# Kernel optimization log

Measured on AMD Instinct MI355X. Metric: run time of the kernel, lower is better.

## Reference

```python
import jax, jax.numpy as jnp
import numpy as np

N = 4096
D = 256
H = 8
HD = D // H
EPS = 1e-5
NEG = -1e9


def layer_norm(x, g, b):
    mu = jnp.mean(x, axis=-1, keepdims=True)
    var = jnp.mean(jnp.square(x - mu), axis=-1, keepdims=True)
    return (x - mu) * jax.lax.rsqrt(var + EPS) * g + b


def setup_inputs() -> dict:
    key = jax.random.key(0)
    ks = jax.random.split(key, 12)
    s = 1.0 / np.sqrt(D)
    inp = {
        "x": jax.random.normal(ks[0], (N, D), dtype=jnp.float32),
        "adj": jax.random.randint(ks[1], (N, N), 0, 2, dtype=jnp.int32),
        "Wq": jax.random.uniform(ks[2], (D, D), jnp.float32, -s, s),
        "Wk": jax.random.uniform(ks[3], (D, D), jnp.float32, -s, s),
        "Wv": jax.random.uniform(ks[4], (D, D), jnp.float32, -s, s),
        "bq": jnp.zeros((D,), jnp.float32),
        "bk": jnp.zeros((D,), jnp.float32),
        "bv": jnp.zeros((D,), jnp.float32),
        "Wo": jax.random.uniform(ks[5], (D, D), jnp.float32, -s, s),
        "bo": jnp.zeros((D,), jnp.float32),
        "g1": jnp.ones((D,), jnp.float32),
        "beta1": jnp.zeros((D,), jnp.float32),
        "W1": jax.random.uniform(ks[6], (2 * D, D), jnp.float32, -s, s),
        "b1": jnp.zeros((2 * D,), jnp.float32),
        "W2": jax.random.uniform(ks[7], (D, 2 * D), jnp.float32, -1.0 / np.sqrt(2 * D), 1.0 / np.sqrt(2 * D)),
        "b2": jnp.zeros((D,), jnp.float32),
        "g2": jnp.ones((D,), jnp.float32),
        "beta2": jnp.zeros((D,), jnp.float32),
    }
    return inp


def reference(x, adj, Wq, Wk, Wv, bq, bk, bv, Wo, bo, g1, beta1, W1, b1, W2, b2, g2, beta2):
    n = adj.shape[0]
    # allowed = adj + I > 0 ; attention only over neighbors + self-loop
    allowed = (adj + jnp.eye(n, dtype=adj.dtype)) > 0  # (n, n) bool

    q = (x @ Wq.T + bq).reshape(n, H, HD)
    k = (x @ Wk.T + bk).reshape(n, H, HD)
    v = (x @ Wv.T + bv).reshape(n, H, HD)

    scale = 1.0 / np.sqrt(HD)
    scores = jnp.einsum('nhd,mhd->hnm', q, k) * scale  # (H, n, n)
    scores = jnp.where(allowed[None, :, :], scores, NEG)
    attn = jax.nn.softmax(scores, axis=-1)
    o = jnp.einsum('hnm,mhd->nhd', attn, v).reshape(n, D)
    h = o @ Wo.T + bo

    x = layer_norm(x + h, g1, beta1)
    ffn = jax.nn.relu(x @ W1.T + b1) @ W2.T + b2
    x = layer_norm(x + ffn, g2, beta2)
    return x
```

## Files before the change

### kernel.cpp

```cpp
#include <hip/hip_runtime.h>
#include <hip/hip_bf16.h>

typedef __attribute__((ext_vector_type(4))) float f32x4;
typedef __attribute__((ext_vector_type(8))) short s16x8;

#define NROWS 4096
#define DMODEL 256
#define NHEAD 8
#define HDIM 32
#define PSTRIDE 72
#define OSTRIDE 33
#define M2C 24.0f
#define NM (NROWS * DMODEL)

__device__ __forceinline__ short bf16r(float f) {
    union { float f; unsigned u; } v; v.f = f;
    unsigned r = v.u + 0x7fffu + ((v.u >> 16) & 1u);
    return (short)(r >> 16);
}

__device__ __forceinline__ float fexp2(float x) {
    float r;
    asm("v_exp_f32 %0, %1" : "=v"(r) : "v"(x));
    return r;
}

__device__ __forceinline__ unsigned pk_bf16(float a, float b) {
#if __has_builtin(__builtin_amdgcn_cvt_pk_bf16_f32)
    typedef __bf16 bf2 __attribute__((ext_vector_type(2)));
    union { bf2 h; unsigned u; } c;
    c.h = __builtin_amdgcn_cvt_pk_bf16_f32(a, b);
    return c.u;
#else
    return (unsigned)(unsigned short)bf16r(a) | ((unsigned)(unsigned short)bf16r(b) << 16);
#endif
}

__device__ __forceinline__ s16x8 pack8(float4 a, float4 b) {
    s16x8 r;
    r[0] = bf16r(a.x); r[1] = bf16r(a.y); r[2] = bf16r(a.z); r[3] = bf16r(a.w);
    r[4] = bf16r(b.x); r[5] = bf16r(b.y); r[6] = bf16r(b.z); r[7] = bf16r(b.w);
    return r;
}

__global__ __launch_bounds__(256) void prep_kernel(const int* __restrict__ adj,
                                                   unsigned* __restrict__ mask,
                                                   const float* __restrict__ Wq,
                                                   const float* __restrict__ Wk,
                                                   const float* __restrict__ Wv,
                                                   const float* __restrict__ Wo,
                                                   const float* __restrict__ W1,
                                                   const float* __restrict__ W2,
                                                   short* __restrict__ wout) {
    const int lane = threadIdx.x & 63;
    if (blockIdx.x < 2048) {
        const int waveid = blockIdx.x * 4 + (threadIdx.x >> 6);
#pragma unroll
        for (int i = 0; i < 32; ++i) {
            const int task = waveid + i * 8192;
            const int row = task >> 6, chunk = task & 63;
            const int c = chunk * 64 + lane;
            int a = adj[(size_t)row * NROWS + c];
            unsigned long long m = __ballot(a > 0 || c == row);
            if (lane == 0)      mask[row * 128 + chunk * 2]     = (unsigned)m;
            else if (lane == 1) mask[row * 128 + chunk * 2 + 1] = (unsigned)(m >> 32);
        }
    } else {
        int i = ((blockIdx.x - 2048) * 256 + threadIdx.x) * 8;
        const float* src; int off;
        if (i < 262144) {
            const float* ws[4] = {Wq, Wk, Wv, Wo};
            src = ws[i >> 16]; off = i & 65535;
        } else if (i < 393216) { src = W1; off = i - 262144; }
        else                   { src = W2; off = i - 393216; }
        float4 a = *(const float4*)(src + off);
        float4 b = *(const float4*)(src + off + 4);
        *(s16x8*)(wout + i) = pack8(a, b);
    }
}

__global__ __launch_bounds__(256) void qkv_kernel(const float* __restrict__ X,
                                                  const short* __restrict__ Wb,
                                                  const float* __restrict__ bq,
                                                  const float* __restrict__ bk,
                                                  const float* __restrict__ bv,
                                                  short* __restrict__ Qb,
                                                  short* __restrict__ Kb,
                                                  short* __restrict__ Vtb) {
    const int tid = threadIdx.x;
    const int wv = tid >> 6, lane = tid & 63;
    const int quad = lane >> 4, col = lane & 15;
    const int n0 = blockIdx.x * 64 + wv * 16;
    const int o0 = blockIdx.y * 64;
    const int z = o0 >> 8;
    const float* bias = (z == 0) ? bq : (z == 1 ? bk : bv);
    const float QSC = 0.25505653437397888f;

    f32x4 zero = {0.f, 0.f, 0.f, 0.f};
    f32x4 acc[4] = {zero, zero, zero, zero};
    const float* ap = X + (size_t)(n0 + col) * DMODEL + quad * 8;
    const short* wp = Wb + (size_t)(o0 + col) * DMODEL + quad * 8;
#pragma unroll
    for (int k0 = 0; k0 < DMODEL; k0 += 32) {
        float4 a0 = *(const float4*)(ap + k0);
        float4 a1 = *(const float4*)(ap + k0 + 4);
        s16x8 af = pack8(a0, a1);
#pragma unroll
        for (int t = 0; t < 4; ++t) {
            s16x8 bf = *(const s16x8*)(wp + (size_t)t * 16 * DMODEL + k0);
            acc[t] = __builtin_amdgcn_mfma_f32_16x16x32_bf16(af, bf, acc[t], 0, 0, 0);
        }
    }
#pragma unroll
    for (int t = 0; t < 4; ++t) {
        const int o = o0 + t * 16 + col;
        const int oo = o & 255;
        float bvv = bias[oo];
#pragma unroll
        for (int r = 0; r < 4; ++r) {
            int n = n0 + quad * 4 + r;
            float v = acc[t][r] + bvv;
            if (z == 0)      Qb[(size_t)n * DMODEL + oo] = bf16r(v * QSC);
            else if (z == 1) Kb[(size_t)(oo >> 5) * NROWS * HDIM + (size_t)n * HDIM + (oo & 31)] = bf16r(v);
            else             Vtb[(size_t)oo * NROWS + n] = bf16r(v);
        }
    }
}

__global__ __launch_bounds__(256) void attn_kernel(const short* __restrict__ Qb,
                                                   const short* __restrict__ Kb,
                                                   const short* __restrict__ Vtb,
                                                   const unsigned* __restrict__ mask,
                                                   float* __restrict__ Opart,
                                                   float* __restrict__ lpart) {
    __shared__ union {
        short sP[2][16 * PSTRIDE];
        float sO[HDIM][OSTRIDE];
    } u[4];
    __shared__ float sl[4][32];

    const int tid = threadIdx.x;
    const int wv = tid >> 6, lane = tid & 63;
    const int quad = lane >> 4, col = lane & 15;
    const int khalf = blockIdx.x & 1;
    const int h = (blockIdx.x >> 1) & 7;
    const int q0 = (blockIdx.x >> 4) * 32;
    const int kw = khalf * 2048 + wv * 512;

    s16x8 qf[2];
    qf[0] = *(const s16x8*)(Qb + (size_t)(q0 + col) * DMODEL + h * HDIM + quad * 8);
    qf[1] = *(const s16x8*)(Qb + (size_t)(q0 + 16 + col) * DMODEL + h * HDIM + quad * 8);

    const short* kp  = Kb + (size_t)h * NROWS * HDIM + (size_t)(kw + col) * HDIM + quad * 8;
    const short* vp0 = Vtb + (size_t)(h * HDIM + col) * NROWS + kw + quad * 8;
    const short* vp1 = vp0 + (size_t)16 * NROWS;
    const unsigned* mp0 = mask + (size_t)(q0 + col) * 128 + (kw >> 5);
    const unsigned* mp1 = mp0 + 16 * 128;

    const short onev = (col == 0) ? (short)0x3F80 : (short)0;
    const s16x8 ones = {onev, onev, onev, onev, onev, onev, onev, onev};

    f32x4 zero = {0.f, 0.f, 0.f, 0.f};
    f32x4 acc[2][2] = {{zero, zero}, {zero, zero}};
    f32x4 lacc[2] = {zero, zero};
    const f32x4 cinit = {-M2C, -M2C, -M2C, -M2C};

    auto loadK = [&](int it, s16x8* kf, uint2* w0, uint2* w1) {
        const short* k = kp + it * 64 * HDIM;
        kf[0] = *(const s16x8*)(k);
        kf[1] = *(const s16x8*)(k + 16 * HDIM);
        kf[2] = *(const s16x8*)(k + 32 * HDIM);
        kf[3] = *(const s16x8*)(k + 48 * HDIM);
        *w0 = *(const uint2*)(mp0 + it * 2);
        *w1 = *(const uint2*)(mp1 + it * 2);
    };

    auto proc = [&](const s16x8* kf, uint2 w0, uint2 w1, int it) {
        const short* v0 = vp0 + it * 64;
        const short* v1 = vp1 + it * 64;
        s16x8 vf00 = *(const s16x8*)(v0);
        s16x8 vf01 = *(const s16x8*)(v0 + 32);
        s16x8 vf10 = *(const s16x8*)(v1);
        s16x8 vf11 = *(const s16x8*)(v1 + 32);
#pragma unroll
        for (int qs = 0; qs < 2; ++qs) {
            unsigned wlo = (qs ? w1.x : w0.x) >> (quad * 4);
            unsigned whi = (qs ? w1.y : w0.y) >> (quad * 4);
            f32x4 st[4];
            st[0] = __builtin_amdgcn_mfma_f32_16x16x32_bf16(kf[0], qf[qs], cinit, 0, 0, 0);
            st[1] = __builtin_amdgcn_mfma_f32_16x16x32_bf16(kf[1], qf[qs], cinit, 0, 0, 0);
            st[2] = __builtin_amdgcn_mfma_f32_16x16x32_bf16(kf[2], qf[qs], cinit, 0, 0, 0);
            st[3] = __builtin_amdgcn_mfma_f32_16x16x32_bf16(kf[3], qf[qs], cinit, 0, 0, 0);

            float p[4][4];
#pragma unroll
            for (int t = 0; t < 4; ++t) {
                unsigned wm = (t < 2) ? wlo : whi;
#pragma unroll
                for (int r = 0; r < 4; ++r) {
                    float e = fexp2(st[t][r]);
                    bool ok = (wm & (1u << ((t & 1) * 16 + r))) != 0u;
                    p[t][r] = ok ? e : 0.f;
                }
            }

            short* pb = &u[wv].sP[qs][0];
#pragma unroll
            for (int t = 0; t < 4; ++t) {
                uint2 pr;
                pr.x = pk_bf16(p[t][0], p[t][1]);
                pr.y = pk_bf16(p[t][2], p[t][3]);
                *(uint2*)(pb + col * PSTRIDE + t * 16 + quad * 4) = pr;
            }
            s16x8 pb0 = *(const s16x8*)(pb + col * PSTRIDE + quad * 8);
            s16x8 pb1 = *(const s16x8*)(pb + col * PSTRIDE + 32 + quad * 8);

            acc[qs][0] = __builtin_amdgcn_mfma_f32_16x16x32_bf16(vf00, pb0, acc[qs][0], 0, 0, 0);
            acc[qs][0] = __builtin_amdgcn_mfma_f32_16x16x32_bf16(vf01, pb1, acc[qs][0], 0, 0, 0);
            acc[qs][1] = __builtin_amdgcn_mfma_f32_16x16x32_bf16(vf10, pb0, acc[qs][1], 0, 0, 0);
            acc[qs][1] = __builtin_amdgcn_mfma_f32_16x16x32_bf16(vf11, pb1, acc[qs][1], 0, 0, 0);
            lacc[qs] = __builtin_amdgcn_mfma_f32_16x16x32_bf16(ones, pb0, lacc[qs], 0, 0, 0);
            lacc[qs] = __builtin_amdgcn_mfma_f32_16x16x32_bf16(ones, pb1, lacc[qs], 0, 0, 0);
        }
    };

    s16x8 kfA[4], kfB[4];
    uint2 w0A, w1A, w0B, w1B;
    loadK(0, kfA, &w0A, &w1A);
    for (int it = 0; it < 8; it += 2) {
        loadK(it + 1, kfB, &w0B, &w1B);
        proc(kfA, w0A, w1A, it);
        if (it < 6) loadK(it + 2, kfA, &w0A, &w1A);
        proc(kfB, w0B, w1B, it + 1);
    }

#pragma unroll
    for (int qs = 0; qs < 2; ++qs) {
        if (lane < 16) sl[wv][qs * 16 + col] = lacc[qs][0];
#pragma unroll
        for (int rr = 0; rr < 4; ++rr) {
            u[wv].sO[quad * 4 + rr][qs * 16 + col]      = acc[qs][0][rr];
            u[wv].sO[16 + quad * 4 + rr][qs * 16 + col] = acc[qs][1][rr];
        }
    }
    __syncthreads();

    const int q = tid >> 3, hd0 = (tid & 7) * 4;
    float l = sl[0][q] + sl[1][q] + sl[2][q] + sl[3][q];
    float4 ov;
    ov.x = u[0].sO[hd0][q]     + u[1].sO[hd0][q]     + u[2].sO[hd0][q]     + u[3].sO[hd0][q];
    ov.y = u[0].sO[hd0 + 1][q] + u[1].sO[hd0 + 1][q] + u[2].sO[hd0 + 1][q] + u[3].sO[hd0 + 1][q];
    ov.z = u[0].sO[hd0 + 2][q] + u[1].sO[hd0 + 2][q] + u[2].sO[hd0 + 2][q] + u[3].sO[hd0 + 2][q];
    ov.w = u[0].sO[hd0 + 3][q] + u[1].sO[hd0 + 3][q] + u[2].sO[hd0 + 3][q] + u[3].sO[hd0 + 3][q];
    *(float4*)(Opart + (size_t)khalf * NM + (size_t)(q0 + q) * DMODEL + h * HDIM + hd0) = ov;
    if ((tid & 7) == 0) lpart[khalf * NROWS * NHEAD + (q0 + q) * NHEAD + h] = l;
}

template<int K, bool RELU, bool B16OUT>
__device__ __forceinline__ void gemm_body(const short* __restrict__ A,
                                          const short* __restrict__ W,
                                          const float* __restrict__ bias,
                                          float* __restrict__ Cf,
                                          short* __restrict__ Cb,
                                          int Ocols) {
    const int tid = threadIdx.x;
    const int wv = tid >> 6, lane = tid & 63;
    const int quad = lane >> 4, col = lane & 15;
    const int n0 = blockIdx.x * 64 + wv * 16;
    const int o0 = blockIdx.y * 64;
    f32x4 zero = {0.f, 0.f, 0.f, 0.f};
    f32x4 acc[4] = {zero, zero, zero, zero};
    const short* ap = A + (size_t)(n0 + col) * K + quad * 8;
    const short* wp = W + (size_t)(o0 + col) * K + quad * 8;
#pragma unroll
    for (int k0 = 0; k0 < K; k0 += 32) {
        s16x8 af = *(const s16x8*)(ap + k0);
#pragma unroll
        for (int t = 0; t < 4; ++t) {
            s16x8 bf = *(const s16x8*)(wp + (size_t)t * 16 * K + k0);
            acc[t] = __builtin_amdgcn_mfma_f32_16x16x32_bf16(af, bf, acc[t], 0, 0, 0);
        }
    }
#pragma unroll
    for (int t = 0; t < 4; ++t) {
        const int o = o0 + t * 16 + col;
        float bvv = bias[o];
#pragma unroll
        for (int r = 0; r < 4; ++r) {
            int n = n0 + quad * 4 + r;
            float v = acc[t][r] + bvv;
            if (RELU) v = fmaxf(v, 0.f);
            if (B16OUT) Cb[(size_t)n * Ocols + o] = bf16r(v);
            else        Cf[(size_t)n * Ocols + o] = v;
        }
    }
}

__global__ __launch_bounds__(256) void gemm_w1(const short* __restrict__ A,
                                               const short* __restrict__ W,
                                               const float* __restrict__ bias,
                                               short* __restrict__ Cb) {
    gemm_body<256, true, true>(A, W, bias, nullptr, Cb, 512);
}

__global__ __launch_bounds__(256) void gemm_w2(const short* __restrict__ A,
                                               const short* __restrict__ W,
                                               const float* __restrict__ bias,
                                               float* __restrict__ Cf) {
    gemm_body<512, false, false>(A, W, bias, Cf, nullptr, 256);
}

__global__ __launch_bounds__(256) void gemm_wo(const float* __restrict__ Opart,
                                               const float* __restrict__ lpart,
                                               const short* __restrict__ W,
                                               const float* __restrict__ bias,
                                               float* __restrict__ Cf) {
    const int tid = threadIdx.x;
    const int wv = tid >> 6, lane = tid & 63;
    const int quad = lane >> 4, col = lane & 15;
    const int n0 = blockIdx.x * 64 + wv * 16;
    const int o0 = blockIdx.y * 64;
    f32x4 zero = {0.f, 0.f, 0.f, 0.f};
    f32x4 acc[4] = {zero, zero, zero, zero};
    const int n = n0 + col;
    const float* a0p = Opart + (size_t)n * DMODEL + quad * 8;
    const float* a1p = a0p + NM;
    const float* l0p = lpart + (size_t)n * NHEAD;
    const float* l1p = l0p + NROWS * NHEAD;
    const short* wp = W + (size_t)(o0 + col) * DMODEL + quad * 8;
#pragma unroll
    for (int k0 = 0; k0 < DMODEL; k0 += 32) {
        const int head = k0 >> 5;
        float inv = 1.f / (l0p[head] + l1p[head]);
        float4 xa = *(const float4*)(a0p + k0);
        float4 xb = *(const float4*)(a0p + k0 + 4);
        float4 ya = *(const float4*)(a1p + k0);
        float4 yb = *(const float4*)(a1p + k0 + 4);
        float4 s0, s1;
        s0.x = (xa.x + ya.x) * inv; s0.y = (xa.y + ya.y) * inv;
        s0.z = (xa.z + ya.z) * inv; s0.w = (xa.w + ya.w) * inv;
        s1.x = (xb.x + yb.x) * inv; s1.y = (xb.y + yb.y) * inv;
        s1.z = (xb.z + yb.z) * inv; s1.w = (xb.w + yb.w) * inv;
        s16x8 af = pack8(s0, s1);
#pragma unroll
        for (int t = 0; t < 4; ++t) {
            s16x8 bf = *(const s16x8*)(wp + (size_t)t * 16 * DMODEL + k0);
            acc[t] = __builtin_amdgcn_mfma_f32_16x16x32_bf16(af, bf, acc[t], 0, 0, 0);
        }
    }
#pragma unroll
    for (int t = 0; t < 4; ++t) {
        const int o = o0 + t * 16 + col;
        float bvv = bias[o];
#pragma unroll
        for (int r = 0; r < 4; ++r)
            Cf[(size_t)(n0 + quad * 4 + r) * DMODEL + o] = acc[t][r] + bvv;
    }
}

__global__ __launch_bounds__(256) void ln_kernel(const float* __restrict__ Xa,
                                                 const float* __restrict__ Xb,
                                                 const float* __restrict__ g,
                                                 const float* __restrict__ be,
                                                 float* __restrict__ Y,
                                                 short* __restrict__ Yb) {
    const int wv = threadIdx.x >> 6, lane = threadIdx.x & 63;
    const int row = blockIdx.x * 4 + wv;
    const float4 av = *(const float4*)(Xa + (size_t)row * DMODEL + lane * 4);
    const float4 bv = *(const float4*)(Xb + (size_t)row * DMODEL + lane * 4);
    float v0 = av.x + bv.x, v1 = av.y + bv.y, v2 = av.z + bv.z, v3 = av.w + bv.w;
    float s = v0 + v1 + v2 + v3;
#pragma unroll
    for (int m = 1; m < 64; m <<= 1) s += __shfl_xor(s, m, 64);
    float mean = s * (1.f / 256.f);
    float d0 = v0 - mean, d1 = v1 - mean, d2 = v2 - mean, d3 = v3 - mean;
    float q = d0 * d0 + d1 * d1 + d2 * d2 + d3 * d3;
#pragma unroll
    for (int m = 1; m < 64; m <<= 1) q += __shfl_xor(q, m, 64);
    float rstd = rsqrtf(q * (1.f / 256.f) + 1e-5f);
    const float4 gv  = *(const float4*)(g + lane * 4);
    const float4 bev = *(const float4*)(be + lane * 4);
    float4 y;
    y.x = d0 * rstd * gv.x + bev.x;
    y.y = d1 * rstd * gv.y + bev.y;
    y.z = d2 * rstd * gv.z + bev.z;
    y.w = d3 * rstd * gv.w + bev.w;
    *(float4*)(Y + (size_t)row * DMODEL + lane * 4) = y;
    if (Yb) {
        uint2 yb;
        yb.x = pk_bf16(y.x, y.y);
        yb.y = pk_bf16(y.z, y.w);
        *(uint2*)(Yb + (size_t)row * DMODEL + lane * 4) = yb;
    }
}

extern "C" void kernel_launch(void* const* d_in, const int* in_sizes, int n_in,
                              void* d_out, int out_size, void* d_ws, size_t ws_size,
                              hipStream_t stream) {
    const float* x   = (const float*)d_in[0];
    const int*   adj = (const int*)d_in[1];
    const float* Wq  = (const float*)d_in[2];
    const float* Wk  = (const float*)d_in[3];
    const float* Wv  = (const float*)d_in[4];
    const float* bq  = (const float*)d_in[5];
    const float* bk  = (const float*)d_in[6];
    const float* bv  = (const float*)d_in[7];
    const float* Wo  = (const float*)d_in[8];
    const float* bo  = (const float*)d_in[9];
    const float* g1  = (const float*)d_in[10];
    const float* be1 = (const float*)d_in[11];
    const float* W1  = (const float*)d_in[12];
    const float* b1  = (const float*)d_in[13];
    const float* W2  = (const float*)d_in[14];
    const float* b2  = (const float*)d_in[15];
    const float* g2  = (const float*)d_in[16];
    const float* be2 = (const float*)d_in[17];
    float* out = (float*)d_out;

    char* p = (char*)d_ws;
    unsigned* mask = (unsigned*)p; p += (size_t)NROWS * 128 * 4;
    short* Wb    = (short*)p;      p += (size_t)524288 * 2;
    short* Qb    = (short*)p;      p += (size_t)NM * 2;
    short* Kb    = (short*)p;      p += (size_t)NM * 2;
    short* Vtb   = (short*)p;      p += (size_t)NM * 2;
    float* Opart = (float*)p;      p += (size_t)2 * NM * 4;
    float* lpart = (float*)p;      p += (size_t)2 * NROWS * NHEAD * 4;
    float* hbuf  = (float*)p;      p += (size_t)NM * 4;
    float* y1    = (float*)p;      p += (size_t)NM * 4;
    short* y1b   = (short*)p;      p += (size_t)NM * 2;
    short* rbuf  = (short*)p;      p += (size_t)NROWS * 512 * 2;
    float* t2    = Opart;

    prep_kernel<<<dim3(2304), dim3(256), 0, stream>>>(adj, mask, Wq, Wk, Wv, Wo, W1, W2, Wb);
    qkv_kernel<<<dim3(64, 12), dim3(256), 0, stream>>>(x, Wb, bq, bk, bv, Qb, Kb, Vtb);
    attn_kernel<<<dim3(2048), dim3(256), 0, stream>>>(Qb, Kb, Vtb, mask, Opart, lpart);
    gemm_wo<<<dim3(64, 4), dim3(256), 0, stream>>>(Opart, lpart, Wb + 196608, bo, hbuf);
    ln_kernel<<<dim3(1024), dim3(256), 0, stream>>>(x, hbuf, g1, be1, y1, y1b);
    gemm_w1<<<dim3(64, 8), dim3(256), 0, stream>>>(y1b, Wb + 262144, b1, rbuf);
    gemm_w2<<<dim3(64, 4), dim3(256), 0, stream>>>(rbuf, Wb + 393216, b2, t2);
    ln_kernel<<<dim3(1024), dim3(256), 0, stream>>>(y1, t2, g2, be2, out, nullptr);
}
```

Measured before the change: 261.1 us.

## Shrink GEMM output tiles to 16 columns for more blocks; simplify attention loop

Measured after the change: 288.9 us. 1.11x slower.

```diff
diff --git a/kernel.cpp b/kernel.cpp
--- a/kernel.cpp
+++ b/kernel.cpp
@@ -90,40 +90,36 @@
     const int tid = threadIdx.x;
     const int wv = tid >> 6, lane = tid & 63;
     const int quad = lane >> 4, col = lane & 15;
-    const int n0 = blockIdx.x * 64 + wv * 16;
-    const int o0 = blockIdx.y * 64;
+    const int n0 = (blockIdx.x * 4 + wv) * 16;
+    const int o0 = blockIdx.y * 16;
     const int z = o0 >> 8;
     const float* bias = (z == 0) ? bq : (z == 1 ? bk : bv);
     const float QSC = 0.25505653437397888f;
 
-    f32x4 zero = {0.f, 0.f, 0.f, 0.f};
-    f32x4 acc[4] = {zero, zero, zero, zero};
+    f32x4 acc0 = {0.f, 0.f, 0.f, 0.f}, acc1 = {0.f, 0.f, 0.f, 0.f};
     const float* ap = X + (size_t)(n0 + col) * DMODEL + quad * 8;
     const short* wp = Wb + (size_t)(o0 + col) * DMODEL + quad * 8;
 #pragma unroll
-    for (int k0 = 0; k0 < DMODEL; k0 += 32) {
+    for (int k0 = 0; k0 < DMODEL; k0 += 64) {
         float4 a0 = *(const float4*)(ap + k0);
         float4 a1 = *(const float4*)(ap + k0 + 4);
-        s16x8 af = pack8(a0, a1);
-#pragma unroll
-        for (int t = 0; t < 4; ++t) {
-            s16x8 bf = *(const s16x8*)(wp + (size_t)t * 16 * DMODEL + k0);
-            acc[t] = __builtin_amdgcn_mfma_f32_16x16x32_bf16(af, bf, acc[t], 0, 0, 0);
-        }
-    }
-#pragma unroll
-    for (int t = 0; t < 4; ++t) {
-        const int o = o0 + t * 16 + col;
-        const int oo = o & 255;
-        float bvv = bias[oo];
-#pragma unroll
-        for (int r = 0; r < 4; ++r) {
-            int n = n0 + quad * 4 + r;
-            float v = acc[t][r] + bvv;
-            if (z == 0)      Qb[(size_t)n * DMODEL + oo] = bf16r(v * QSC);
-            else if (z == 1) Kb[(size_t)(oo >> 5) * NROWS * HDIM + (size_t)n * HDIM + (oo & 31)] = bf16r(v);
-            else             Vtb[(size_t)oo * NROWS + n] = bf16r(v);
-        }
+        float4 a2 = *(const float4*)(ap + k0 + 32);
+        float4 a3 = *(const float4*)(ap + k0 + 36);
+        s16x8 b0 = *(const s16x8*)(wp + k0);
+        s16x8 b1 = *(const s16x8*)(wp + k0 + 32);
+        acc0 = __builtin_amdgcn_mfma_f32_16x16x32_bf16(pack8(a0, a1), b0, acc0, 0, 0, 0);
+        acc1 = __builtin_amdgcn_mfma_f32_16x16x32_bf16(pack8(a2, a3), b1, acc1, 0, 0, 0);
+    }
+    const int o = o0 + col;
+    const int oo = o & 255;
+    float bvv = bias[oo];
+#pragma unroll
+    for (int r = 0; r < 4; ++r) {
+        int n = n0 + quad * 4 + r;
+        float v = acc0[r] + acc1[r] + bvv;
+        if (z == 0)      Qb[(size_t)n * DMODEL + oo] = bf16r(v * QSC);
+        else if (z == 1) Kb[(size_t)(oo >> 5) * NROWS * HDIM + (size_t)n * HDIM + (oo & 31)] = bf16r(v);
+        else             Vtb[(size_t)oo * NROWS + n] = bf16r(v);
     }
 }
 
@@ -165,32 +161,31 @@
     f32x4 lacc[2] = {zero, zero};
     const f32x4 cinit = {-M2C, -M2C, -M2C, -M2C};
 
-    auto loadK = [&](int it, s16x8* kf, uint2* w0, uint2* w1) {
+#pragma unroll 2
+    for (int it = 0; it < 8; ++it) {
         const short* k = kp + it * 64 * HDIM;
-        kf[0] = *(const s16x8*)(k);
-        kf[1] = *(const s16x8*)(k + 16 * HDIM);
-        kf[2] = *(const s16x8*)(k + 32 * HDIM);
-        kf[3] = *(const s16x8*)(k + 48 * HDIM);
-        *w0 = *(const uint2*)(mp0 + it * 2);
-        *w1 = *(const uint2*)(mp1 + it * 2);
-    };
-
-    auto proc = [&](const s16x8* kf, uint2 w0, uint2 w1, int it) {
+        s16x8 kf0 = *(const s16x8*)(k);
+        s16x8 kf1 = *(const s16x8*)(k + 16 * HDIM);
+        s16x8 kf2 = *(const s16x8*)(k + 32 * HDIM);
+        s16x8 kf3 = *(const s16x8*)(k + 48 * HDIM);
+        uint2 w0 = *(const uint2*)(mp0 + it * 2);
+        uint2 w1 = *(const uint2*)(mp1 + it * 2);
         const short* v0 = vp0 + it * 64;
         const short* v1 = vp1 + it * 64;
         s16x8 vf00 = *(const s16x8*)(v0);
         s16x8 vf01 = *(const s16x8*)(v0 + 32);
         s16x8 vf10 = *(const s16x8*)(v1);
         s16x8 vf11 = *(const s16x8*)(v1 + 32);
+
 #pragma unroll
         for (int qs = 0; qs < 2; ++qs) {
             unsigned wlo = (qs ? w1.x : w0.x) >> (quad * 4);
             unsigned whi = (qs ? w1.y : w0.y) >> (quad * 4);
             f32x4 st[4];
-            st[0] = __builtin_amdgcn_mfma_f32_16x16x32_bf16(kf[0], qf[qs], cinit, 0, 0, 0);
-            st[1] = __builtin_amdgcn_mfma_f32_16x16x32_bf16(kf[1], qf[qs], cinit, 0, 0, 0);
-            st[2] = __builtin_amdgcn_mfma_f32_16x16x32_bf16(kf[2], qf[qs], cinit, 0, 0, 0);
-            st[3] = __builtin_amdgcn_mfma_f32_16x16x32_bf16(kf[3], qf[qs], cinit, 0, 0, 0);
+            st[0] = __builtin_amdgcn_mfma_f32_16x16x32_bf16(kf0, qf[qs], cinit, 0, 0, 0);
+            st[1] = __builtin_amdgcn_mfma_f32_16x16x32_bf16(kf1, qf[qs], cinit, 0, 0, 0);
+            st[2] = __builtin_amdgcn_mfma_f32_16x16x32_bf16(kf2, qf[qs], cinit, 0, 0, 0);
+            st[3] = __builtin_amdgcn_mfma_f32_16x16x32_bf16(kf3, qf[qs], cinit, 0, 0, 0);
 
             float p[4][4];
 #pragma unroll
@@ -222,16 +217,6 @@
             lacc[qs] = __builtin_amdgcn_mfma_f32_16x16x32_bf16(ones, pb0, lacc[qs], 0, 0, 0);
             lacc[qs] = __builtin_amdgcn_mfma_f32_16x16x32_bf16(ones, pb1, lacc[qs], 0, 0, 0);
         }
-    };
-
-    s16x8 kfA[4], kfB[4];
-    uint2 w0A, w1A, w0B, w1B;
-    loadK(0, kfA, &w0A, &w1A);
-    for (int it = 0; it < 8; it += 2) {
-        loadK(it + 1, kfB, &w0B, &w1B);
-        proc(kfA, w0A, w1A, it);
-        if (it < 6) loadK(it + 2, kfA, &w0A, &w1A);
-        proc(kfB, w0B, w1B, it + 1);
     }
 
 #pragma unroll
@@ -257,42 +242,38 @@
 }
 
 template<int K, bool RELU, bool B16OUT>
-__device__ __forceinline__ void gemm_body(const short* __restrict__ A,
-                                          const short* __restrict__ W,
-                                          const float* __restrict__ bias,
-                                          float* __restrict__ Cf,
-                                          short* __restrict__ Cb,
-                                          int Ocols) {
+__device__ __forceinline__ void gemm16_body(const short* __restrict__ A,
+                                            const short* __restrict__ W,
+                                            const float* __restrict__ bias,
+                                            float* __restrict__ Cf,
+                                            short* __restrict__ Cb,
+                                            int Ocols) {
     const int tid = threadIdx.x;
     const int wv = tid >> 6, lane = tid & 63;
     const int quad = lane >> 4, col = lane & 15;
-    const int n0 = blockIdx.x * 64 + wv * 16;
-    const int o0 = blockIdx.y * 64;
-    f32x4 zero = {0.f, 0.f, 0.f, 0.f};
-    f32x4 acc[4] = {zero, zero, zero, zero};
+    const int n0 = (blockIdx.x * 4 + wv) * 16;
+    const int o0 = blockIdx.y * 16;
+    f32x4 acc0 = {0.f, 0.f, 0.f, 0.f}, acc1 = {0.f, 0.f, 0.f, 0.f};
     const short* ap = A + (size_t)(n0 + col) * K + quad * 8;
     const short* wp = W + (size_t)(o0 + col) * K + quad * 8;
 #pragma unroll
-    for (int k0 = 0; k0 < K; k0 += 32) {
-        s16x8 af = *(const s16x8*)(ap + k0);
-#pragma unroll
-        for (int t = 0; t < 4; ++t) {
-            s16x8 bf = *(const s16x8*)(wp + (size_t)t * 16 * K + k0);
-            acc[t] = __builtin_amdgcn_mfma_f32_16x16x32_bf16(af, bf, acc[t], 0, 0, 0);
-        }
-    }
-#pragma unroll
-    for (int t = 0; t < 4; ++t) {
-        const int o = o0 + t * 16 + col;
-        float bvv = bias[o];
-#pragma unroll
-        for (int r = 0; r < 4; ++r) {
-            int n = n0 + quad * 4 + r;
-            float v = acc[t][r] + bvv;
-            if (RELU) v = fmaxf(v, 0.f);
-            if (B16OUT) Cb[(size_t)n * Ocols + o] = bf16r(v);
-            else        Cf[(size_t)n * Ocols + o] = v;
-        }
+    for (int k0 = 0; k0 < K; k0 += 64) {
+        s16x8 a0 = *(const s16x8*)(ap + k0);
+        s16x8 b0 = *(const s16x8*)(wp + k0);
+        s16x8 a1 = *(const s16x8*)(ap + k0 + 32);
+        s16x8 b1 = *(const s16x8*)(wp + k0 + 32);
+        acc0 = __builtin_amdgcn_mfma_f32_16x16x32_bf16(a0, b0, acc0, 0, 0, 0);
+        acc1 = __builtin_amdgcn_mfma_f32_16x16x32_bf16(a1, b1, acc1, 0, 0, 0);
+    }
+    const int o = o0 + col;
+    float bvv = bias[o];
+#pragma unroll
+    for (int r = 0; r < 4; ++r) {
+        int n = n0 + quad * 4 + r;
+        float v = acc0[r] + acc1[r] + bvv;
+        if (RELU) v = fmaxf(v, 0.f);
+        if (B16OUT) Cb[(size_t)n * Ocols + o] = bf16r(v);
+        else        Cf[(size_t)n * Ocols + o] = v;
     }
 }
 
@@ -300,14 +281,14 @@
                                                const short* __restrict__ W,
                                                const float* __restrict__ bias,
                                                short* __restrict__ Cb) {
-    gemm_body<256, true, true>(A, W, bias, nullptr, Cb, 512);
+    gemm16_body<256, true, true>(A, W, bias, nullptr, Cb, 512);
 }
 
 __global__ __launch_bounds__(256) void gemm_w2(const short* __restrict__ A,
                                                const short* __restrict__ W,
                                                const float* __restrict__ bias,
                                                float* __restrict__ Cf) {
-    gemm_body<512, false, false>(A, W, bias, Cf, nullptr, 256);
+    gemm16_body<512, false, false>(A, W, bias, Cf, nullptr, 256);
 }
 
 __global__ __launch_bounds__(256) void gemm_wo(const float* __restrict__ Opart,
@@ -318,10 +299,9 @@
     const int tid = threadIdx.x;
     const int wv = tid >> 6, lane = tid & 63;
     const int quad = lane >> 4, col = lane & 15;
-    const int n0 = blockIdx.x * 64 + wv * 16;
-    const int o0 = blockIdx.y * 64;
-    f32x4 zero = {0.f, 0.f, 0.f, 0.f};
-    f32x4 acc[4] = {zero, zero, zero, zero};
+    const int n0 = (blockIdx.x * 4 + wv) * 16;
+    const int o0 = blockIdx.y * 16;
+    f32x4 acc0 = {0.f, 0.f, 0.f, 0.f}, acc1 = {0.f, 0.f, 0.f, 0.f};
     const int n = n0 + col;
     const float* a0p = Opart + (size_t)n * DMODEL + quad * 8;
     const float* a1p = a0p + NM;
@@ -342,20 +322,15 @@
         s1.x = (xb.x + yb.x) * inv; s1.y = (xb.y + yb.y) * inv;
         s1.z = (xb.z + yb.z) * inv; s1.w = (xb.w + yb.w) * inv;
         s16x8 af = pack8(s0, s1);
-#pragma unroll
-        for (int t = 0; t < 4; ++t) {
-            s16x8 bf = *(const s16x8*)(wp + (size_t)t * 16 * DMODEL + k0);
-            acc[t] = __builtin_amdgcn_mfma_f32_16x16x32_bf16(af, bf, acc[t], 0, 0, 0);
-        }
-    }
-#pragma unroll
-    for (int t = 0; t < 4; ++t) {
-        const int o = o0 + t * 16 + col;
-        float bvv = bias[o];
-#pragma unroll
-        for (int r = 0; r < 4; ++r)
-            Cf[(size_t)(n0 + quad * 4 + r) * DMODEL + o] = acc[t][r] + bvv;
-    }
+        s16x8 bf = *(const s16x8*)(wp + k0);
+        if (head & 1) acc1 = __builtin_amdgcn_mfma_f32_16x16x32_bf16(af, bf, acc1, 0, 0, 0);
+        else          acc0 = __builtin_amdgcn_mfma_f32_16x16x32_bf16(af, bf, acc0, 0, 0, 0);
+    }
+    const int o = o0 + col;
+    float bvv = bias[o];
+#pragma unroll
+    for (int r = 0; r < 4; ++r)
+        Cf[(size_t)(n0 + quad * 4 + r) * DMODEL + o] = acc0[r] + acc1[r] + bvv;
 }
 
 __global__ __launch_bounds__(256) void ln_kernel(const float* __restrict__ Xa,
@@ -432,11 +407,11 @@
     float* t2    = Opart;
 
     prep_kernel<<<dim3(2304), dim3(256), 0, stream>>>(adj, mask, Wq, Wk, Wv, Wo, W1, W2, Wb);
-    qkv_kernel<<<dim3(64, 12), dim3(256), 0, stream>>>(x, Wb, bq, bk, bv, Qb, Kb, Vtb);
+    qkv_kernel<<<dim3(64, 48), dim3(256), 0, stream>>>(x, Wb, bq, bk, bv, Qb, Kb, Vtb);
     attn_kernel<<<dim3(2048), dim3(256), 0, stream>>>(Qb, Kb, Vtb, mask, Opart, lpart);
-    gemm_wo<<<dim3(64, 4), dim3(256), 0, stream>>>(Opart, lpart, Wb + 196608, bo, hbuf);
+    gemm_wo<<<dim3(64, 16), dim3(256), 0, stream>>>(Opart, lpart, Wb + 196608, bo, hbuf);
     ln_kernel<<<dim3(1024), dim3(256), 0, stream>>>(x, hbuf, g1, be1, y1, y1b);
-    gemm_w1<<<dim3(64, 8), dim3(256), 0, stream>>>(y1b, Wb + 262144, b1, rbuf);
-    gemm_w2<<<dim3(64, 4), dim3(256), 0, stream>>>(rbuf, Wb + 393216, b2, t2);
+    gemm_w1<<<dim3(64, 32), dim3(256), 0, stream>>>(y1b, Wb + 262144, b1, rbuf);
+    gemm_w2<<<dim3(64, 16), dim3(256), 0, stream>>>(rbuf, Wb + 393216, b2, t2);
     ln_kernel<<<dim3(1024), dim3(256), 0, stream>>>(y1, t2, g2, be2, out, nullptr);
 }
```

## Fuse post-attention GEMMs and layernorms into one kernel; merge QKV with prep

Applied to the files above, without the earlier changes.

New measurement: 240.8 us. -7.8%, faster.

```diff
diff --git a/kernel.cpp b/kernel.cpp
--- a/kernel.cpp
+++ b/kernel.cpp
@@ -12,6 +12,10 @@
 #define OSTRIDE 33
 #define M2C 24.0f
 #define NM (NROWS * DMODEL)
+#define SA_S 264
+#define SH_S 268
+#define SY_S 264
+#define SR_S 520
 
 __device__ __forceinline__ short bf16r(float f) {
     union { float f; unsigned u; } v; v.f = f;
@@ -43,18 +47,62 @@
     return r;
 }
 
-__global__ __launch_bounds__(256) void prep_kernel(const int* __restrict__ adj,
-                                                   unsigned* __restrict__ mask,
-                                                   const float* __restrict__ Wq,
-                                                   const float* __restrict__ Wk,
-                                                   const float* __restrict__ Wv,
-                                                   const float* __restrict__ Wo,
-                                                   const float* __restrict__ W1,
-                                                   const float* __restrict__ W2,
-                                                   short* __restrict__ wout) {
-    const int lane = threadIdx.x & 63;
-    if (blockIdx.x < 2048) {
-        const int waveid = blockIdx.x * 4 + (threadIdx.x >> 6);
+__global__ __launch_bounds__(256) void qkvprep_kernel(
+        const float* __restrict__ X,
+        const float* __restrict__ Wq, const float* __restrict__ Wk,
+        const float* __restrict__ Wv,
+        const float* __restrict__ bq, const float* __restrict__ bk,
+        const float* __restrict__ bv,
+        const int* __restrict__ adj, unsigned* __restrict__ mask,
+        const float* __restrict__ Wo, const float* __restrict__ W1,
+        const float* __restrict__ W2, short* __restrict__ Wb,
+        short* __restrict__ Qb, short* __restrict__ Kb,
+        short* __restrict__ Vtb) {
+    const int b = blockIdx.x;
+    const int tid = threadIdx.x;
+    const int lane = tid & 63;
+    if (b < 768) {
+        const int wv = tid >> 6;
+        const int quad = lane >> 4, col = lane & 15;
+        const int bx = b & 63, by = b >> 6;
+        const int o0 = by * 64;
+        const int z = o0 >> 8;
+        const float* Wsrc = (z == 0) ? Wq : (z == 1 ? Wk : Wv);
+        const float* bias = (z == 0) ? bq : (z == 1 ? bk : bv);
+        const int ow0 = o0 & 255;
+        const int n0 = bx * 64 + wv * 16;
+        const float QSC = 0.25505653437397888f;
+
+        f32x4 zero = {0.f, 0.f, 0.f, 0.f};
+        f32x4 acc[4] = {zero, zero, zero, zero};
+        const float* ap = X + (size_t)(n0 + col) * DMODEL + quad * 8;
+#pragma unroll
+        for (int k0 = 0; k0 < DMODEL; k0 += 32) {
+            float4 a0 = *(const float4*)(ap + k0);
+            float4 a1 = *(const float4*)(ap + k0 + 4);
+            s16x8 af = pack8(a0, a1);
+#pragma unroll
+            for (int t = 0; t < 4; ++t) {
+                const float* wp = Wsrc + (size_t)(ow0 + t * 16 + col) * DMODEL + quad * 8 + k0;
+                s16x8 bf = pack8(*(const float4*)wp, *(const float4*)(wp + 4));
+                acc[t] = __builtin_amdgcn_mfma_f32_16x16x32_bf16(af, bf, acc[t], 0, 0, 0);
+            }
+        }
+#pragma unroll
+        for (int t = 0; t < 4; ++t) {
+            const int oo = ow0 + t * 16 + col;
+            float bvv = bias[oo];
+#pragma unroll
+            for (int r = 0; r < 4; ++r) {
+                int n = n0 + quad * 4 + r;
+                float v = acc[t][r] + bvv;
+                if (z == 0)      Qb[(size_t)n * DMODEL + oo] = bf16r(v * QSC);
+                else if (z == 1) Kb[(size_t)(oo >> 5) * NROWS * HDIM + (size_t)n * HDIM + (oo & 31)] = bf16r(v);
+                else             Vtb[(size_t)oo * NROWS + n] = bf16r(v);
+            }
+        }
+    } else if (b < 2816) {
+        const int waveid = (b - 768) * 4 + (tid >> 6);
 #pragma unroll
         for (int i = 0; i < 32; ++i) {
             const int task = waveid + i * 8192;
@@ -66,64 +114,14 @@
             else if (lane == 1) mask[row * 128 + chunk * 2 + 1] = (unsigned)(m >> 32);
         }
     } else {
-        int i = ((blockIdx.x - 2048) * 256 + threadIdx.x) * 8;
+        int i = (b - 2816) * 2048 + tid * 8;
         const float* src; int off;
-        if (i < 262144) {
-            const float* ws[4] = {Wq, Wk, Wv, Wo};
-            src = ws[i >> 16]; off = i & 65535;
-        } else if (i < 393216) { src = W1; off = i - 262144; }
-        else                   { src = W2; off = i - 393216; }
+        if (i < 65536)       { src = Wo; off = i; }
+        else if (i < 196608) { src = W1; off = i - 65536; }
+        else                 { src = W2; off = i - 196608; }
         float4 a = *(const float4*)(src + off);
-        float4 b = *(const float4*)(src + off + 4);
-        *(s16x8*)(wout + i) = pack8(a, b);
-    }
-}
-
-__global__ __launch_bounds__(256) void qkv_kernel(const float* __restrict__ X,
-                                                  const short* __restrict__ Wb,
-                                                  const float* __restrict__ bq,
-                                                  const float* __restrict__ bk,
-                                                  const float* __restrict__ bv,
-                                                  short* __restrict__ Qb,
-                                                  short* __restrict__ Kb,
-                                                  short* __restrict__ Vtb) {
-    const int tid = threadIdx.x;
-    const int wv = tid >> 6, lane = tid & 63;
-    const int quad = lane >> 4, col = lane & 15;
-    const int n0 = blockIdx.x * 64 + wv * 16;
-    const int o0 = blockIdx.y * 64;
-    const int z = o0 >> 8;
-    const float* bias = (z == 0) ? bq : (z == 1 ? bk : bv);
-    const float QSC = 0.25505653437397888f;
-
-    f32x4 zero = {0.f, 0.f, 0.f, 0.f};
-    f32x4 acc[4] = {zero, zero, zero, zero};
-    const float* ap = X + (size_t)(n0 + col) * DMODEL + quad * 8;
-    const short* wp = Wb + (size_t)(o0 + col) * DMODEL + quad * 8;
-#pragma unroll
-    for (int k0 = 0; k0 < DMODEL; k0 += 32) {
-        float4 a0 = *(const float4*)(ap + k0);
-        float4 a1 = *(const float4*)(ap + k0 + 4);
-        s16x8 af = pack8(a0, a1);
-#pragma unroll
-        for (int t = 0; t < 4; ++t) {
-            s16x8 bf = *(const s16x8*)(wp + (size_t)t * 16 * DMODEL + k0);
-            acc[t] = __builtin_amdgcn_mfma_f32_16x16x32_bf16(af, bf, acc[t], 0, 0, 0);
-        }
-    }
-#pragma unroll
-    for (int t = 0; t < 4; ++t) {
-        const int o = o0 + t * 16 + col;
-        const int oo = o & 255;
-        float bvv = bias[oo];
-#pragma unroll
-        for (int r = 0; r < 4; ++r) {
-            int n = n0 + quad * 4 + r;
-            float v = acc[t][r] + bvv;
-            if (z == 0)      Qb[(size_t)n * DMODEL + oo] = bf16r(v * QSC);
-            else if (z == 1) Kb[(size_t)(oo >> 5) * NROWS * HDIM + (size_t)n * HDIM + (oo & 31)] = bf16r(v);
-            else             Vtb[(size_t)oo * NROWS + n] = bf16r(v);
-        }
+        float4 c = *(const float4*)(src + off + 4);
+        *(s16x8*)(Wb + i) = pack8(a, c);
     }
 }
 
@@ -165,32 +163,31 @@
     f32x4 lacc[2] = {zero, zero};
     const f32x4 cinit = {-M2C, -M2C, -M2C, -M2C};
 
-    auto loadK = [&](int it, s16x8* kf, uint2* w0, uint2* w1) {
+#pragma unroll 2
+    for (int it = 0; it < 8; ++it) {
         const short* k = kp + it * 64 * HDIM;
-        kf[0] = *(const s16x8*)(k);
-        kf[1] = *(const s16x8*)(k + 16 * HDIM);
-        kf[2] = *(const s16x8*)(k + 32 * HDIM);
-        kf[3] = *(const s16x8*)(k + 48 * HDIM);
-        *w0 = *(const uint2*)(mp0 + it * 2);
-        *w1 = *(const uint2*)(mp1 + it * 2);
-    };
-
-    auto proc = [&](const s16x8* kf, uint2 w0, uint2 w1, int it) {
+        s16x8 kf0 = *(const s16x8*)(k);
+        s16x8 kf1 = *(const s16x8*)(k + 16 * HDIM);
+        s16x8 kf2 = *(const s16x8*)(k + 32 * HDIM);
+        s16x8 kf3 = *(const s16x8*)(k + 48 * HDIM);
+        uint2 w0 = *(const uint2*)(mp0 + it * 2);
+        uint2 w1 = *(const uint2*)(mp1 + it * 2);
         const short* v0 = vp0 + it * 64;
         const short* v1 = vp1 + it * 64;
         s16x8 vf00 = *(const s16x8*)(v0);
         s16x8 vf01 = *(const s16x8*)(v0 + 32);
         s16x8 vf10 = *(const s16x8*)(v1);
         s16x8 vf11 = *(const s16x8*)(v1 + 32);
+
 #pragma unroll
         for (int qs = 0; qs < 2; ++qs) {
             unsigned wlo = (qs ? w1.x : w0.x) >> (quad * 4);
             unsigned whi = (qs ? w1.y : w0.y) >> (quad * 4);
             f32x4 st[4];
-            st[0] = __builtin_amdgcn_mfma_f32_16x16x32_bf16(kf[0], qf[qs], cinit, 0, 0, 0);
-            st[1] = __builtin_amdgcn_mfma_f32_16x16x32_bf16(kf[1], qf[qs], cinit, 0, 0, 0);
-            st[2] = __builtin_amdgcn_mfma_f32_16x16x32_bf16(kf[2], qf[qs], cinit, 0, 0, 0);
-            st[3] = __builtin_amdgcn_mfma_f32_16x16x32_bf16(kf[3], qf[qs], cinit, 0, 0, 0);
+            st[0] = __builtin_amdgcn_mfma_f32_16x16x32_bf16(kf0, qf[qs], cinit, 0, 0, 0);
+            st[1] = __builtin_amdgcn_mfma_f32_16x16x32_bf16(kf1, qf[qs], cinit, 0, 0, 0);
+            st[2] = __builtin_amdgcn_mfma_f32_16x16x32_bf16(kf2, qf[qs], cinit, 0, 0, 0);
+            st[3] = __builtin_amdgcn_mfma_f32_16x16x32_bf16(kf3, qf[qs], cinit, 0, 0, 0);
 
             float p[4][4];
 #pragma unroll
@@ -222,16 +219,6 @@
             lacc[qs] = __builtin_amdgcn_mfma_f32_16x16x32_bf16(ones, pb0, lacc[qs], 0, 0, 0);
             lacc[qs] = __builtin_amdgcn_mfma_f32_16x16x32_bf16(ones, pb1, lacc[qs], 0, 0, 0);
         }
-    };
-
-    s16x8 kfA[4], kfB[4];
-    uint2 w0A, w1A, w0B, w1B;
-    loadK(0, kfA, &w0A, &w1A);
-    for (int it = 0; it < 8; it += 2) {
-        loadK(it + 1, kfB, &w0B, &w1B);
-        proc(kfA, w0A, w1A, it);
-        if (it < 6) loadK(it + 2, kfA, &w0A, &w1A);
-        proc(kfB, w0B, w1B, it + 1);
     }
 
 #pragma unroll
@@ -256,141 +243,192 @@
     if ((tid & 7) == 0) lpart[khalf * NROWS * NHEAD + (q0 + q) * NHEAD + h] = l;
 }
 
-template<int K, bool RELU, bool B16OUT>
-__device__ __forceinline__ void gemm_body(const short* __restrict__ A,
-                                          const short* __restrict__ W,
-                                          const float* __restrict__ bias,
-                                          float* __restrict__ Cf,
-                                          short* __restrict__ Cb,
-                                          int Ocols) {
+__global__ __launch_bounds__(256) void mega_kernel(
+        const float* __restrict__ Opart, const float* __restrict__ lpart,
+        const float* __restrict__ X,
+        const short* __restrict__ Wob, const short* __restrict__ W1b,
+        const short* __restrict__ W2b,
+        const float* __restrict__ bo,
+        const float* __restrict__ g1, const float* __restrict__ be1,
+        const float* __restrict__ b1, const float* __restrict__ b2,
+        const float* __restrict__ g2, const float* __restrict__ be2,
+        float* __restrict__ out) {
+    __shared__ union { short sA[16 * SA_S]; short sR[16 * SR_S]; } uu;
+    __shared__ float sH[16 * SH_S];
+    __shared__ short sY[16 * SY_S];
+
     const int tid = threadIdx.x;
     const int wv = tid >> 6, lane = tid & 63;
     const int quad = lane >> 4, col = lane & 15;
-    const int n0 = blockIdx.x * 64 + wv * 16;
-    const int o0 = blockIdx.y * 64;
+    const int n0 = blockIdx.x * 16;
+    const int rr_ = tid >> 4, cg = tid & 15;
+    const int n_ln = n0 + rr_;
     f32x4 zero = {0.f, 0.f, 0.f, 0.f};
-    f32x4 acc[4] = {zero, zero, zero, zero};
-    const short* ap = A + (size_t)(n0 + col) * K + quad * 8;
-    const short* wp = W + (size_t)(o0 + col) * K + quad * 8;
-#pragma unroll
-    for (int k0 = 0; k0 < K; k0 += 32) {
-        s16x8 af = *(const s16x8*)(ap + k0);
+
+    {
+        const int head = cg >> 1;
+        float li = 1.f / (lpart[(size_t)n_ln * NHEAD + head] +
+                          lpart[(size_t)NROWS * NHEAD + (size_t)n_ln * NHEAD + head]);
+        const float* p0 = Opart + (size_t)n_ln * DMODEL + cg * 16;
+        const float* p1 = p0 + NM;
+        short* dst = &uu.sA[rr_ * SA_S + cg * 16];
+#pragma unroll
+        for (int j = 0; j < 4; ++j) {
+            float4 a = ((const float4*)p0)[j];
+            float4 b = ((const float4*)p1)[j];
+            uint2 w;
+            w.x = pk_bf16((a.x + b.x) * li, (a.y + b.y) * li);
+            w.y = pk_bf16((a.z + b.z) * li, (a.w + b.w) * li);
+            *(uint2*)(dst + j * 4) = w;
+        }
+    }
+    __syncthreads();
+
+    {
+        const int o0 = wv * 64;
+        f32x4 acc[4] = {zero, zero, zero, zero};
+#pragma unroll
+        for (int k0 = 0; k0 < DMODEL; k0 += 32) {
+            s16x8 af = *(const s16x8*)&uu.sA[col * SA_S + k0 + quad * 8];
+#pragma unroll
+            for (int t = 0; t < 4; ++t) {
+                s16x8 bf = *(const s16x8*)(Wob + (size_t)(o0 + t * 16 + col) * DMODEL + k0 + quad * 8);
+                acc[t] = __builtin_amdgcn_mfma_f32_16x16x32_bf16(af, bf, acc[t], 0, 0, 0);
+            }
+        }
 #pragma unroll
         for (int t = 0; t < 4; ++t) {
-            s16x8 bf = *(const s16x8*)(wp + (size_t)t * 16 * K + k0);
-            acc[t] = __builtin_amdgcn_mfma_f32_16x16x32_bf16(af, bf, acc[t], 0, 0, 0);
-        }
-    }
-#pragma unroll
-    for (int t = 0; t < 4; ++t) {
-        const int o = o0 + t * 16 + col;
-        float bvv = bias[o];
-#pragma unroll
-        for (int r = 0; r < 4; ++r) {
-            int n = n0 + quad * 4 + r;
-            float v = acc[t][r] + bvv;
-            if (RELU) v = fmaxf(v, 0.f);
-            if (B16OUT) Cb[(size_t)n * Ocols + o] = bf16r(v);
-            else        Cf[(size_t)n * Ocols + o] = v;
-        }
-    }
-}
-
-__global__ __launch_bounds__(256) void gemm_w1(const short* __restrict__ A,
-                                               const short* __restrict__ W,
-                                               const float* __restrict__ bias,
-                                               short* __restrict__ Cb) {
-    gemm_body<256, true, true>(A, W, bias, nullptr, Cb, 512);
-}
-
-__global__ __launch_bounds__(256) void gemm_w2(const short* __restrict__ A,
-                                               const short* __restrict__ W,
-                                               const float* __restrict__ bias,
-                                               float* __restrict__ Cf) {
-    gemm_body<512, false, false>(A, W, bias, Cf, nullptr, 256);
-}
-
-__global__ __launch_bounds__(256) void gemm_wo(const float* __restrict__ Opart,
-                                               const float* __restrict__ lpart,
-                                               const short* __restrict__ W,
-                                               const float* __restrict__ bias,
-                                               float* __restrict__ Cf) {
-    const int tid = threadIdx.x;
-    const int wv = tid >> 6, lane = tid & 63;
-    const int quad = lane >> 4, col = lane & 15;
-    const int n0 = blockIdx.x * 64 + wv * 16;
-    const int o0 = blockIdx.y * 64;
-    f32x4 zero = {0.f, 0.f, 0.f, 0.f};
-    f32x4 acc[4] = {zero, zero, zero, zero};
-    const int n = n0 + col;
-    const float* a0p = Opart + (size_t)n * DMODEL + quad * 8;
-    const float* a1p = a0p + NM;
-    const float* l0p = lpart + (size_t)n * NHEAD;
-    const float* l1p = l0p + NROWS * NHEAD;
-    const short* wp = W + (size_t)(o0 + col) * DMODEL + quad * 8;
-#pragma unroll
-    for (int k0 = 0; k0 < DMODEL; k0 += 32) {
-        const int head = k0 >> 5;
-        float inv = 1.f / (l0p[head] + l1p[head]);
-        float4 xa = *(const float4*)(a0p + k0);
-        float4 xb = *(const float4*)(a0p + k0 + 4);
-        float4 ya = *(const float4*)(a1p + k0);
-        float4 yb = *(const float4*)(a1p + k0 + 4);
-        float4 s0, s1;
-        s0.x = (xa.x + ya.x) * inv; s0.y = (xa.y + ya.y) * inv;
-        s0.z = (xa.z + ya.z) * inv; s0.w = (xa.w + ya.w) * inv;
-        s1.x = (xb.x + yb.x) * inv; s1.y = (xb.y + yb.y) * inv;
-        s1.z = (xb.z + yb.z) * inv; s1.w = (xb.w + yb.w) * inv;
-        s16x8 af = pack8(s0, s1);
+            int o = o0 + t * 16 + col;
+            float bv = bo[o];
+#pragma unroll
+            for (int r = 0; r < 4; ++r)
+                sH[(quad * 4 + r) * SH_S + o] = acc[t][r] + bv;
+        }
+    }
+    __syncthreads();
+
+    float y1v[16];
+    {
+        const float* xp = X + (size_t)n_ln * DMODEL + cg * 16;
+        float v[16];
+        float s = 0.f;
+#pragma unroll
+        for (int j = 0; j < 4; ++j) {
+            float4 xv = ((const float4*)xp)[j];
+            float4 hv = *(const float4*)&sH[rr_ * SH_S + cg * 16 + j * 4];
+            v[j * 4 + 0] = xv.x + hv.x; v[j * 4 + 1] = xv.y + hv.y;
+            v[j * 4 + 2] = xv.z + hv.z; v[j * 4 + 3] = xv.w + hv.w;
+            s += v[j * 4] + v[j * 4 + 1] + v[j * 4 + 2] + v[j * 4 + 3];
+        }
+#pragma unroll
+        for (int m = 1; m < 16; m <<= 1) s += __shfl_xor(s, m, 64);
+        float mean = s * (1.f / 256.f);
+        float q = 0.f;
+#pragma unroll
+        for (int i = 0; i < 16; ++i) { v[i] -= mean; q += v[i] * v[i]; }
+#pragma unroll
+        for (int m = 1; m < 16; m <<= 1) q += __shfl_xor(q, m, 64);
+        float rstd = rsqrtf(q * (1.f / 256.f) + 1e-5f);
+        const float* gp = g1 + cg * 16;
+        const float* bp = be1 + cg * 16;
+        short* dst = &sY[rr_ * SY_S + cg * 16];
+#pragma unroll
+        for (int j = 0; j < 4; ++j) {
+            float4 gv = ((const float4*)gp)[j];
+            float4 bev = ((const float4*)bp)[j];
+            float a0 = v[j * 4 + 0] * rstd * gv.x + bev.x;
+            float a1 = v[j * 4 + 1] * rstd * gv.y + bev.y;
+            float a2 = v[j * 4 + 2] * rstd * gv.z + bev.z;
+            float a3 = v[j * 4 + 3] * rstd * gv.w + bev.w;
+            y1v[j * 4 + 0] = a0; y1v[j * 4 + 1] = a1;
+            y1v[j * 4 + 2] = a2; y1v[j * 4 + 3] = a3;
+            uint2 w;
+            w.x = pk_bf16(a0, a1);
+            w.y = pk_bf16(a2, a3);
+            *(uint2*)(dst + j * 4) = w;
+        }
+    }
+    __syncthreads();
+
+    {
+        const int o0 = wv * 128;
+        f32x4 acc[8] = {zero, zero, zero, zero, zero, zero, zero, zero};
+#pragma unroll
+        for (int k0 = 0; k0 < DMODEL; k0 += 32) {
+            s16x8 af = *(const s16x8*)&sY[col * SY_S + k0 + quad * 8];
+#pragma unroll
+            for (int t = 0; t < 8; ++t) {
+                s16x8 bf = *(const s16x8*)(W1b + (size_t)(o0 + t * 16 + col) * DMODEL + k0 + quad * 8);
+                acc[t] = __builtin_amdgcn_mfma_f32_16x16x32_bf16(af, bf, acc[t], 0, 0, 0);
+            }
+        }
+#pragma unroll
+        for (int t = 0; t < 8; ++t) {
+            int o = o0 + t * 16 + col;
+            float bv = b1[o];
+#pragma unroll
+            for (int r = 0; r < 4; ++r)
+                uu.sR[(quad * 4 + r) * SR_S + o] = bf16r(fmaxf(acc[t][r] + bv, 0.f));
+        }
+    }
+    __syncthreads();
+
+    {
+        const int o0 = wv * 64;
+        f32x4 acc[4] = {zero, zero, zero, zero};
+#pragma unroll
+        for (int k0 = 0; k0 < 512; k0 += 32) {
+            s16x8 af = *(const s16x8*)&uu.sR[col * SR_S + k0 + quad * 8];
+#pragma unroll
+            for (int t = 0; t < 4; ++t) {
+                s16x8 bf = *(const s16x8*)(W2b + (size_t)(o0 + t * 16 + col) * 512 + k0 + quad * 8);
+                acc[t] = __builtin_amdgcn_mfma_f32_16x16x32_bf16(af, bf, acc[t], 0, 0, 0);
+            }
+        }
 #pragma unroll
         for (int t = 0; t < 4; ++t) {
-            s16x8 bf = *(const s16x8*)(wp + (size_t)t * 16 * DMODEL + k0);
-            acc[t] = __builtin_amdgcn_mfma_f32_16x16x32_bf16(af, bf, acc[t], 0, 0, 0);
-        }
-    }
-#pragma unroll
-    for (int t = 0; t < 4; ++t) {
-        const int o = o0 + t * 16 + col;
-        float bvv = bias[o];
-#pragma unroll
-        for (int r = 0; r < 4; ++r)
-            Cf[(size_t)(n0 + quad * 4 + r) * DMODEL + o] = acc[t][r] + bvv;
-    }
-}
-
-__global__ __launch_bounds__(256) void ln_kernel(const float* __restrict__ Xa,
-                                                 const float* __restrict__ Xb,
-                                                 const float* __restrict__ g,
-                                                 const float* __restrict__ be,
-                                                 float* __restrict__ Y,
-                                                 short* __restrict__ Yb) {
-    const int wv = threadIdx.x >> 6, lane = threadIdx.x & 63;
-    const int row = blockIdx.x * 4 + wv;
-    const float4 av = *(const float4*)(Xa + (size_t)row * DMODEL + lane * 4);
-    const float4 bv = *(const float4*)(Xb + (size_t)row * DMODEL + lane * 4);
-    float v0 = av.x + bv.x, v1 = av.y + bv.y, v2 = av.z + bv.z, v3 = av.w + bv.w;
-    float s = v0 + v1 + v2 + v3;
-#pragma unroll
-    for (int m = 1; m < 64; m <<= 1) s += __shfl_xor(s, m, 64);
-    float mean = s * (1.f / 256.f);
-    float d0 = v0 - mean, d1 = v1 - mean, d2 = v2 - mean, d3 = v3 - mean;
-    float q = d0 * d0 + d1 * d1 + d2 * d2 + d3 * d3;
-#pragma unroll
-    for (int m = 1; m < 64; m <<= 1) q += __shfl_xor(q, m, 64);
-    float rstd = rsqrtf(q * (1.f / 256.f) + 1e-5f);
-    const float4 gv  = *(const float4*)(g + lane * 4);
-    const float4 bev = *(const float4*)(be + lane * 4);
-    float4 y;
-    y.x = d0 * rstd * gv.x + bev.x;
-    y.y = d1 * rstd * gv.y + bev.y;
-    y.z = d2 * rstd * gv.z + bev.z;
-    y.w = d3 * rstd * gv.w + bev.w;
-    *(float4*)(Y + (size_t)row * DMODEL + lane * 4) = y;
-    if (Yb) {
-        uint2 yb;
-        yb.x = pk_bf16(y.x, y.y);
-        yb.y = pk_bf16(y.z, y.w);
-        *(uint2*)(Yb + (size_t)row * DMODEL + lane * 4) = yb;
+            int o = o0 + t * 16 + col;
+            float bv = b2[o];
+#pragma unroll
+            for (int r = 0; r < 4; ++r)
+                sH[(quad * 4 + r) * SH_S + o] = acc[t][r] + bv;
+        }
+    }
+    __syncthreads();
+
+    {
+        float v[16];
+        float s = 0.f;
+#pragma unroll
+        for (int j = 0; j < 4; ++j) {
+            float4 hv = *(const float4*)&sH[rr_ * SH_S + cg * 16 + j * 4];
+            v[j * 4 + 0] = y1v[j * 4 + 0] + hv.x; v[j * 4 + 1] = y1v[j * 4 + 1] + hv.y;
+            v[j * 4 + 2] = y1v[j * 4 + 2] + hv.z; v[j * 4 + 3] = y1v[j * 4 + 3] + hv.w;
+            s += v[j * 4] + v[j * 4 + 1] + v[j * 4 + 2] + v[j * 4 + 3];
+        }
+#pragma unroll
+        for (int m = 1; m < 16; m <<= 1) s += __shfl_xor(s, m, 64);
+        float mean = s * (1.f / 256.f);
+        float q = 0.f;
+#pragma unroll
+        for (int i = 0; i < 16; ++i) { v[i] -= mean; q += v[i] * v[i]; }
+#pragma unroll
+        for (int m = 1; m < 16; m <<= 1) q += __shfl_xor(q, m, 64);
+        float rstd = rsqrtf(q * (1.f / 256.f) + 1e-5f);
+        const float* gp = g2 + cg * 16;
+        const float* bp = be2 + cg * 16;
+        float* op = out + (size_t)n_ln * DMODEL + cg * 16;
+#pragma unroll
+        for (int j = 0; j < 4; ++j) {
+            float4 gv = ((const float4*)gp)[j];
+            float4 bev = ((const float4*)bp)[j];
+            float4 y;
+            y.x = v[j * 4 + 0] * rstd * gv.x + bev.x;
+            y.y = v[j * 4 + 1] * rstd * gv.y + bev.y;
+            y.z = v[j * 4 + 2] * rstd * gv.z + bev.z;
+            y.w = v[j * 4 + 3] * rstd * gv.w + bev.w;
+            ((float4*)op)[j] = y;
+        }
     }
 }
 
@@ -419,24 +457,17 @@
 
     char* p = (char*)d_ws;
     unsigned* mask = (unsigned*)p; p += (size_t)NROWS * 128 * 4;
-    short* Wb    = (short*)p;      p += (size_t)524288 * 2;
+    short* Wb    = (short*)p;      p += (size_t)327680 * 2;
     short* Qb    = (short*)p;      p += (size_t)NM * 2;
     short* Kb    = (short*)p;      p += (size_t)NM * 2;
     short* Vtb   = (short*)p;      p += (size_t)NM * 2;
     float* Opart = (float*)p;      p += (size_t)2 * NM * 4;
     float* lpart = (float*)p;      p += (size_t)2 * NROWS * NHEAD * 4;
-    float* hbuf  = (float*)p;      p += (size_t)NM * 4;
-    float* y1    = (float*)p;      p += (size_t)NM * 4;
-    short* y1b   = (short*)p;      p += (size_t)NM * 2;
-    short* rbuf  = (short*)p;      p += (size_t)NROWS * 512 * 2;
-    float* t2    = Opart;
-
-    prep_kernel<<<dim3(2304), dim3(256), 0, stream>>>(adj, mask, Wq, Wk, Wv, Wo, W1, W2, Wb);
-    qkv_kernel<<<dim3(64, 12), dim3(256), 0, stream>>>(x, Wb, bq, bk, bv, Qb, Kb, Vtb);
+
+    qkvprep_kernel<<<dim3(2976), dim3(256), 0, stream>>>(
+        x, Wq, Wk, Wv, bq, bk, bv, adj, mask, Wo, W1, W2, Wb, Qb, Kb, Vtb);
     attn_kernel<<<dim3(2048), dim3(256), 0, stream>>>(Qb, Kb, Vtb, mask, Opart, lpart);
-    gemm_wo<<<dim3(64, 4), dim3(256), 0, stream>>>(Opart, lpart, Wb + 196608, bo, hbuf);
-    ln_kernel<<<dim3(1024), dim3(256), 0, stream>>>(x, hbuf, g1, be1, y1, y1b);
-    gemm_w1<<<dim3(64, 8), dim3(256), 0, stream>>>(y1b, Wb + 262144, b1, rbuf);
-    gemm_w2<<<dim3(64, 4), dim3(256), 0, stream>>>(rbuf, Wb + 393216, b2, t2);
-    ln_kernel<<<dim3(1024), dim3(256), 0, stream>>>(y1, t2, g2, be2, out, nullptr);
-}
+    mega_kernel<<<dim3(256), dim3(256), 0, stream>>>(
+        Opart, lpart, x, Wb, Wb + 65536, Wb + 196608,
+        bo, g1, be1, b1, b2, g2, be2, out);
+}
```
